# Kernel optimization log

Measured on AMD Instinct MI355X. Metric: run time of the kernel, lower is better.

Reference implementation:

```python
import jax, jax.numpy as jnp
import numpy as np

B, S, H = 2, 2048, 2048
NH, HD = 16, 128


def _rope_tables(seq_len, dim, base=10000.0):
    inv_freq = 1.0 / (base ** (np.arange(0, dim, 2, dtype=np.float32) / dim))
    t = np.arange(seq_len, dtype=np.float32)
    freqs = np.outer(t, inv_freq)                      # [S, dim/2]
    emb = np.concatenate([freqs, freqs], axis=-1)      # [S, dim] (HF convention)
    return jnp.asarray(np.cos(emb)), jnp.asarray(np.sin(emb))


def setup_inputs() -> dict:
    key = jax.random.key(0)
    k1, k2, k3, k4, k5 = jax.random.split(key, 5)
    hidden_states = jax.random.normal(k1, (B, S, H), dtype=jnp.float32)
    # additive causal mask, broadcast over heads: (B, 1, S, S)
    causal = jnp.tril(jnp.ones((S, S), dtype=bool))
    attention_mask = jnp.where(causal, 0.0, -1e9).astype(jnp.float32)
    attention_mask = jnp.broadcast_to(attention_mask[None, None], (B, 1, S, S))
    rope_cos, rope_sin = _rope_tables(S, HD)
    scale = 1.0 / np.sqrt(H)
    Wq = jax.random.normal(k2, (H, H), dtype=jnp.float32) * scale
    Wk = jax.random.normal(k3, (H, H), dtype=jnp.float32) * scale
    Wv = jax.random.normal(k4, (H, H), dtype=jnp.float32) * scale
    Wo = jax.random.normal(k5, (H, H), dtype=jnp.float32) * scale
    return dict(hidden_states=hidden_states, attention_mask=attention_mask,
                rope_cos=rope_cos, rope_sin=rope_sin, Wq=Wq, Wk=Wk, Wv=Wv, Wo=Wo)


def _rotate_half(x):
    half = x.shape[-1] // 2
    return jnp.concatenate([-x[..., half:], x[..., :half]], axis=-1)


def reference(hidden_states, attention_mask, rope_cos, rope_sin, Wq, Wk, Wv, Wo):
    bsz, q_len, _ = hidden_states.shape
    scaling = HD ** -0.5
    # projections (torch Linear: y = x @ W.T)
    q = (hidden_states @ Wq.T).reshape(bsz, q_len, NH, HD).transpose(0, 2, 1, 3)
    k = (hidden_states @ Wk.T).reshape(bsz, q_len, NH, HD).transpose(0, 2, 1, 3)
    v = (hidden_states @ Wv.T).reshape(bsz, q_len, NH, HD).transpose(0, 2, 1, 3)
    # RoPE (rotate_half convention)
    cos = rope_cos[None, None]  # [1,1,S,HD]
    sin = rope_sin[None, None]
    q = q * cos + _rotate_half(q) * sin
    k = k * cos + _rotate_half(k) * sin
    # attention
    scores = jnp.einsum('bhqd,bhkd->bhqk', q, k) * scaling + attention_mask
    attn = jax.nn.softmax(scores.astype(jnp.float32), axis=-1).astype(q.dtype)
    out = jnp.einsum('bhqk,bhkd->bhqd', attn, v)
    out = out.transpose(0, 2, 1, 3).reshape(bsz, q_len, NH * HD)
    return out @ Wo.T
```

## Files before the change

kernel.cpp:

```cpp
#include <hip/hip_runtime.h>
#include <hip/hip_bf16.h>

typedef __bf16 bf16;
typedef __attribute__((ext_vector_type(8))) __bf16 bf16x8;
typedef __attribute__((ext_vector_type(4))) __bf16 bf16x4;
typedef __attribute__((ext_vector_type(4))) float f32x4;

#define BB 2
#define SS 2048
#define HH 2048
#define NH 16
#define HD 128

#define GLOAD_LDS16(g, l)                                                  \
    __builtin_amdgcn_global_load_lds(                                      \
        (const __attribute__((address_space(1))) void*)(g),                \
        (__attribute__((address_space(3))) void*)(l), 16, 0, 0)

__global__ __launch_bounds__(256) void cast_f32_bf16(const float* __restrict__ in,
                                                     bf16* __restrict__ out, int n4) {
    int i = blockIdx.x * 256 + threadIdx.x;
    if (i < n4) {
        f32x4 v = *reinterpret_cast<const f32x4*>(in + (size_t)i * 4);
        bf16x4 o;
        o[0] = (bf16)v[0]; o[1] = (bf16)v[1]; o[2] = (bf16)v[2]; o[3] = (bf16)v[3];
        *reinterpret_cast<bf16x4*>(out + (size_t)i * 4) = o;
    }
}

__global__ __launch_bounds__(512, 2) void gemm256_qkv(const bf16* __restrict__ A,
                                                      const bf16* __restrict__ B,
                                                      bf16* __restrict__ Cb,
                                                      int M, int N, int K) {
    __shared__ bf16 LA[2][256 * 64];
    __shared__ bf16 LB[2][256 * 64];
    const int tid = threadIdx.x, lane = tid & 63, wave = tid >> 6;
    const int l15 = lane & 15, lhi = lane >> 4;
    const int wr = wave >> 2, wc = wave & 3;
    const int NBX = N >> 8;
    const int cpx = gridDim.x >> 3;
    const int wg = (blockIdx.x & 7) * cpx + (blockIdx.x >> 3);
    const int m0 = (wg / NBX) * 256, n0 = (wg % NBX) * 256;
    const int NK = K >> 6;
    const int xor5 = (l15 & 8) << 2;

    auto stageA = [&](int buf, int t, int h) {
        const int k0 = t << 6;
#pragma unroll
        for (int j = 0; j < 2; ++j) {
            int Xw = ((j * 128 + h * 64) << 7) + (wave << 10);
            int X = Xw + lane * 16;
            int T = X ^ (((X >> 10) & 1) << 5);
            GLOAD_LDS16(&A[(size_t)(m0 + (T >> 7)) * K + k0 + ((T & 127) >> 1)],
                        (char*)LA[buf] + Xw);
        }
    };
    auto stageB = [&](int buf, int t, int h) {
        const int k0 = t << 6;
#pragma unroll
        for (int j = 0; j < 2; ++j) {
            int base_row = h * 32 + (2 * j + (wave >> 2)) * 64;
            int Xw = (base_row << 7) + ((wave & 3) << 10);
            int X = Xw + lane * 16;
            int T = X ^ (((X >> 10) & 1) << 5);
            GLOAD_LDS16(&B[(size_t)(n0 + (T >> 7)) * K + k0 + ((T & 127) >> 1)],
                        (char*)LB[buf] + Xw);
        }
    };

    f32x4 acc[8][4] = {};

    stageA(0, 0, 0); stageB(0, 0, 0); stageB(0, 0, 1); stageA(0, 0, 1);
    stageA(1, 1, 0); stageB(1, 1, 1);
    asm volatile("s_waitcnt vmcnt(4)" ::: "memory");
    __builtin_amdgcn_s_barrier();

    bf16x8 af[4][2], bv0[2][2], bv1[2][2];

#pragma unroll 1
    for (int t = 0; t < NK; ++t) {
        const int buf = t & 1;
        char* lA = (char*)LA[buf];
        char* lB = (char*)LB[buf];

#pragma unroll
        for (int f = 0; f < 4; ++f)
#pragma unroll
            for (int ks = 0; ks < 2; ++ks) {
                int T = ((wr * 128 + f * 16 + l15) << 7) + ks * 64 + lhi * 16;
                af[f][ks] = *reinterpret_cast<const bf16x8*>(lA + (T ^ xor5));
            }
#pragma unroll
        for (int g = 0; g < 2; ++g)
#pragma unroll
            for (int ks = 0; ks < 2; ++ks) {
                int T = ((wc * 64 + g * 16 + l15) << 7) + ks * 64 + lhi * 16;
                bv0[g][ks] = *reinterpret_cast<const bf16x8*>(lB + (T ^ xor5));
            }
        if (t + 1 < NK) stageB(buf ^ 1, t + 1, 0);
        __builtin_amdgcn_s_barrier();
        asm volatile("s_waitcnt lgkmcnt(0)" ::: "memory");
        __builtin_amdgcn_s_setprio(1);
#pragma unroll
        for (int f = 0; f < 4; ++f)
#pragma unroll
            for (int g = 0; g < 2; ++g)
#pragma unroll
                for (int ks = 0; ks < 2; ++ks)
                    acc[f][g] = __builtin_amdgcn_mfma_f32_16x16x32_bf16(af[f][ks], bv0[g][ks], acc[f][g], 0, 0, 0);
        __builtin_amdgcn_s_setprio(0);
        __builtin_amdgcn_s_barrier();

#pragma unroll
        for (int g = 0; g < 2; ++g)
#pragma unroll
            for (int ks = 0; ks < 2; ++ks) {
                int T = ((wc * 64 + 32 + g * 16 + l15) << 7) + ks * 64 + lhi * 16;
                bv1[g][ks] = *reinterpret_cast<const bf16x8*>(lB + (T ^ xor5));
            }
        if (t + 1 < NK) stageA(buf ^ 1, t + 1, 1);
        __builtin_amdgcn_s_barrier();
        asm volatile("s_waitcnt lgkmcnt(0)" ::: "memory");
        __builtin_amdgcn_s_setprio(1);
#pragma unroll
        for (int f = 0; f < 4; ++f)
#pragma unroll
            for (int g = 0; g < 2; ++g)
#pragma unroll
                for (int ks = 0; ks < 2; ++ks)
                    acc[f][2 + g] = __builtin_amdgcn_mfma_f32_16x16x32_bf16(af[f][ks], bv1[g][ks], acc[f][2 + g], 0, 0, 0);
        __builtin_amdgcn_s_setprio(0);
        __builtin_amdgcn_s_barrier();

#pragma unroll
        for (int f = 0; f < 4; ++f)
#pragma unroll
            for (int ks = 0; ks < 2; ++ks) {
                int T = ((wr * 128 + 64 + f * 16 + l15) << 7) + ks * 64 + lhi * 16;
                af[f][ks] = *reinterpret_cast<const bf16x8*>(lA + (T ^ xor5));
            }
        if (t + 2 < NK) stageA(buf, t + 2, 0);
        __builtin_amdgcn_s_barrier();
        asm volatile("s_waitcnt lgkmcnt(0)" ::: "memory");
        __builtin_amdgcn_s_setprio(1);
#pragma unroll
        for (int f = 0; f < 4; ++f)
#pragma unroll
            for (int g = 0; g < 2; ++g)
#pragma unroll
                for (int ks = 0; ks < 2; ++ks)
                    acc[4 + f][2 + g] = __builtin_amdgcn_mfma_f32_16x16x32_bf16(af[f][ks], bv1[g][ks], acc[4 + f][2 + g], 0, 0, 0);
        __builtin_amdgcn_s_setprio(0);
        __builtin_amdgcn_s_barrier();

        if (t + 2 < NK) stageB(buf, t + 2, 1);
        __builtin_amdgcn_s_barrier();
        __builtin_amdgcn_s_setprio(1);
#pragma unroll
        for (int f = 0; f < 4; ++f)
#pragma unroll
            for (int g = 0; g < 2; ++g)
#pragma unroll
                for (int ks = 0; ks < 2; ++ks)
                    acc[4 + f][g] = __builtin_amdgcn_mfma_f32_16x16x32_bf16(af[f][ks], bv0[g][ks], acc[4 + f][g], 0, 0, 0);
        __builtin_amdgcn_s_setprio(0);
        if (t + 2 == NK) {
            asm volatile("s_waitcnt vmcnt(0)" ::: "memory");
        } else if (t + 1 < NK) {
            asm volatile("s_waitcnt vmcnt(4)" ::: "memory");
        }
        __builtin_amdgcn_s_barrier();
    }

#pragma unroll
    for (int mf = 0; mf < 8; ++mf)
#pragma unroll
        for (int nf = 0; nf < 4; ++nf)
#pragma unroll
            for (int r = 0; r < 4; ++r) {
                int gm = m0 + wr * 128 + mf * 16 + lhi * 4 + r;
                int gn = n0 + wc * 64 + nf * 16 + l15;
                int proj = gn >> 11, n2 = gn & 2047;
                int b = gm >> 11, s = gm & (SS - 1);
                int h = n2 >> 7, d = n2 & (HD - 1);
                Cb[((size_t)proj << 23) + ((((size_t)(b * NH + h)) * SS + s) << 7) + d] =
                    (bf16)acc[mf][nf][r];
            }
}

__global__ __launch_bounds__(256) void gemm_bt(const bf16* __restrict__ A,
                                               const bf16* __restrict__ B,
                                               float* __restrict__ Cf,
                                               int M, int N, int K) {
    __shared__ bf16 As[128 * 64];
    __shared__ bf16 Bs[128 * 64];
    const int tid = threadIdx.x;
    const int lane = tid & 63, wave = tid >> 6;
    const int l15 = lane & 15, lhi = lane >> 4;
    const int m0 = blockIdx.y * 128, n0 = blockIdx.x * 128;
    const int wm = (wave >> 1) * 64, wn = (wave & 1) * 64;
    const int lrow = lane >> 3;
    const int lcol = (lane & 7) * 8;

    f32x4 acc[4][4] = {};

    for (int k0 = 0; k0 < K; k0 += 64) {
#pragma unroll
        for (int j = 0; j < 4; ++j) {
            const int c = wave * 4 + j;
            const int row = c * 8 + lrow;
            GLOAD_LDS16(&A[(size_t)(m0 + row) * K + k0 + lcol], &As[c * 512]);
            GLOAD_LDS16(&B[(size_t)(n0 + row) * K + k0 + lcol], &Bs[c * 512]);
        }
        __syncthreads();
#pragma unroll
        for (int ks = 0; ks < 2; ++ks) {
            bf16x8 af[4], bfr[4];
#pragma unroll
            for (int i = 0; i < 4; ++i)
                af[i] = *reinterpret_cast<const bf16x8*>(&As[(wm + i * 16 + l15) * 64 + ks * 32 + 8 * lhi]);
#pragma unroll
            for (int j = 0; j < 4; ++j)
                bfr[j] = *reinterpret_cast<const bf16x8*>(&Bs[(wn + j * 16 + l15) * 64 + ks * 32 + 8 * lhi]);
#pragma unroll
            for (int i = 0; i < 4; ++i)
#pragma unroll
                for (int j = 0; j < 4; ++j)
                    acc[i][j] = __builtin_amdgcn_mfma_f32_16x16x32_bf16(af[i], bfr[j], acc[i][j], 0, 0, 0);
        }
        __syncthreads();
    }

#pragma unroll
    for (int i = 0; i < 4; ++i)
#pragma unroll
        for (int j = 0; j < 4; ++j)
#pragma unroll
            for (int r = 0; r < 4; ++r) {
                int gm = m0 + wm + i * 16 + lhi * 4 + r;
                int gn = n0 + wn + j * 16 + l15;
                Cf[(size_t)gm * N + gn] = acc[i][j][r];
            }
}

__global__ __launch_bounds__(256) void transpose_v(const bf16* __restrict__ Vh,
                                                   bf16* __restrict__ Vt) {
    __shared__ bf16 T[64 * 64];
    const int tid = threadIdx.x;
    const int s0 = blockIdx.x * 64, d0 = blockIdx.y * 64, head = blockIdx.z;
    const bf16* src = Vh + ((size_t)head * SS) * HD;
    bf16* dst = Vt + ((size_t)head * HD) * SS;

#pragma unroll
    for (int i = 0; i < 2; ++i) {
        int id = tid + i * 256;
        int r = id >> 3, c16 = id & 7;
        bf16x8 v = *reinterpret_cast<const bf16x8*>(&src[(size_t)(s0 + r) * HD + d0 + c16 * 8]);
        int sw = c16 ^ ((r ^ (r >> 3)) & 7);
        *reinterpret_cast<bf16x8*>((char*)T + r * 128 + sw * 16) = v;
    }
    __syncthreads();
#pragma unroll
    for (int i = 0; i < 2; ++i) {
        int id = tid + i * 256;
        int dr = id >> 3, sc8 = (id & 7) * 8;
        bf16x8 o;
#pragma unroll
        for (int j = 0; j < 8; ++j) {
            int r = sc8 + j;
            int sw = (dr >> 3) ^ ((r ^ (r >> 3)) & 7);
            o[j] = *reinterpret_cast<const bf16*>((char*)T + r * 128 + sw * 16 + (dr & 7) * 2);
        }
        *reinterpret_cast<bf16x8*>(&dst[(size_t)(d0 + dr) * SS + s0 + sc8]) = o;
    }
}

__global__ __launch_bounds__(256) void rope_kernel(bf16* __restrict__ Qh, bf16* __restrict__ Kh,
                                                   const float* __restrict__ cosT,
                                                   const float* __restrict__ sinT) {
    int idx = blockIdx.x * 256 + threadIdx.x;
    int g = idx & 7;
    int s = (idx >> 3) & (SS - 1);
    int head = idx >> 14;
    int d0 = g * 8;
    size_t base = ((size_t)head * SS + s) * HD;
    f32x4 ca = *reinterpret_cast<const f32x4*>(&cosT[s * HD + d0]);
    f32x4 cb = *reinterpret_cast<const f32x4*>(&cosT[s * HD + d0 + 4]);
    f32x4 sa = *reinterpret_cast<const f32x4*>(&sinT[s * HD + d0]);
    f32x4 sb = *reinterpret_cast<const f32x4*>(&sinT[s * HD + d0 + 4]);
    bf16x8 ql = *reinterpret_cast<const bf16x8*>(&Qh[base + d0]);
    bf16x8 qh = *reinterpret_cast<const bf16x8*>(&Qh[base + 64 + d0]);
    bf16x8 kl = *reinterpret_cast<const bf16x8*>(&Kh[base + d0]);
    bf16x8 kh = *reinterpret_cast<const bf16x8*>(&Kh[base + 64 + d0]);
    bf16x8 qlo, qhi, klo, khi;
#pragma unroll
    for (int j = 0; j < 8; ++j) {
        float c = (j < 4) ? ca[j] : cb[j - 4];
        float sn = (j < 4) ? sa[j] : sb[j - 4];
        float q0 = (float)ql[j], q1 = (float)qh[j];
        float k0 = (float)kl[j], k1 = (float)kh[j];
        qlo[j] = (bf16)(q0 * c - q1 * sn);
        qhi[j] = (bf16)(q1 * c + q0 * sn);
        klo[j] = (bf16)(k0 * c - k1 * sn);
        khi[j] = (bf16)(k1 * c + k0 * sn);
    }
    *reinterpret_cast<bf16x8*>(&Qh[base + d0]) = qlo;
    *reinterpret_cast<bf16x8*>(&Qh[base + 64 + d0]) = qhi;
    *reinterpret_cast<bf16x8*>(&Kh[base + d0]) = klo;
    *reinterpret_cast<bf16x8*>(&Kh[base + 64 + d0]) = khi;
}

__global__ __launch_bounds__(256) void attn_kernel(const bf16* __restrict__ Q,
                                                   const bf16* __restrict__ K,
                                                   const bf16* __restrict__ Vt,
                                                   bf16* __restrict__ Ob) {
    __shared__ bf16 Ks[2][64 * 128];
    __shared__ bf16 Vs[2][128 * 64];
    __shared__ bf16 Ps[4][16][72];

    const int tid = threadIdx.x, lane = tid & 63, wave = tid >> 6;
    const int l15 = lane & 15, lhi = lane >> 4;
    const int bid = blockIdx.x;
    const int orig = (bid & 7) * 64 + (bid >> 3);
    const int head = orig >> 4;
    const int pi = orig & 15;
    const int b = head >> 4, h = head & (NH - 1);
    const size_t hb = (size_t)head * SS * HD;
    const bf16* Vth = Vt + (size_t)head * HD * SS;
    const float cexp = 0.08838834764831845f * 1.4426950408889634f;
    const float THR = 62.0f;

#pragma unroll 1
    for (int part = 0; part < 2; ++part) {
        const int t = part ? (31 - pi) : pi;
        const int q0 = t * 64;
        const int qw = q0 + wave * 16;
        const int nkv = t + 1;

        bf16x8 qf[4];
#pragma unroll
        for (int ks = 0; ks < 4; ++ks)
            qf[ks] = *reinterpret_cast<const bf16x8*>(
                &Q[hb + (size_t)(qw + l15) * HD + ks * 32 + 8 * lhi]);

        f32x4 oacc[8] = {};
        float Mr[4], Lp[4];
#pragma unroll
        for (int r = 0; r < 4; ++r) { Mr[r] = -INFINITY; Lp[r] = 0.f; }

        bf16x8 kr[4], vr[4];
#pragma unroll
        for (int i = 0; i < 4; ++i) {
            int id = tid + i * 256;
            kr[i] = *reinterpret_cast<const bf16x8*>(&K[hb + (size_t)(id >> 4) * HD + (id & 15) * 8]);
            vr[i] = *reinterpret_cast<const bf16x8*>(&Vth[(size_t)(id >> 3) * SS + (id & 7) * 8]);
        }
#pragma unroll
        for (int i = 0; i < 4; ++i) {
            int id = tid + i * 256;
            int krow = id >> 4, kc = id & 15;
            *reinterpret_cast<bf16x8*>((char*)Ks[0] + ((krow * 256 + kc * 16) ^ ((krow & 7) << 4))) = kr[i];
            int vrow = id >> 3, vc = id & 7;
            *reinterpret_cast<bf16x8*>((char*)Vs[0] + ((vrow * 128 + vc * 16) ^ ((vrow & 7) << 4))) = vr[i];
        }
        __syncthreads();

        for (int it = 0; it < nkv; ++it) {
            const int cur = it & 1;
            const bool pre = (it + 1 < nkv);
            if (pre) {
                const int kv0 = (it + 1) * 64;
#pragma unroll
                for (int i = 0; i < 4; ++i) {
                    int id = tid + i * 256;
                    kr[i] = *reinterpret_cast<const bf16x8*>(&K[hb + (size_t)(kv0 + (id >> 4)) * HD + (id & 15) * 8]);
                    vr[i] = *reinterpret_cast<const bf16x8*>(&Vth[(size_t)(id >> 3) * SS + kv0 + (id & 7) * 8]);
                }
            }

            f32x4 sf[4] = {};
#pragma unroll
            for (int ks = 0; ks < 4; ++ks) {
#pragma unroll
                for (int ne = 0; ne < 4; ++ne) {
                    int row = ne * 16 + l15;
                    bf16x8 kf = *reinterpret_cast<const bf16x8*>(
                        (const char*)Ks[cur] + ((row * 256 + (ks * 4 + lhi) * 16) ^ ((row & 7) << 4)));
                    sf[ne] = __builtin_amdgcn_mfma_f32_16x16x32_bf16(qf[ks], kf, sf[ne], 0, 0, 0);
                }
            }

            if (it == nkv - 1) {
#pragma unroll
                for (int ne = 0; ne < 4; ++ne)
#pragma unroll
                    for (int r = 0; r < 4; ++r) {
                        int gq = qw + lhi * 4 + r;
                        int gk = it * 64 + ne * 16 + l15;
                        if (gk > gq) sf[ne][r] = -INFINITY;
                    }
            }

            float lm[4];
#pragma unroll
            for (int r = 0; r < 4; ++r)
                lm[r] = fmaxf(fmaxf(sf[0][r], sf[1][r]), fmaxf(sf[2][r], sf[3][r]));
            bool need = (lm[0] > Mr[0] + THR) || (lm[1] > Mr[1] + THR) ||
                        (lm[2] > Mr[2] + THR) || (lm[3] > Mr[3] + THR);
            if (__any(need)) {
                float rmax[4] = {lm[0], lm[1], lm[2], lm[3]};
#pragma unroll
                for (int m = 1; m < 16; m <<= 1)
#pragma unroll
                    for (int r = 0; r < 4; ++r)
                        rmax[r] = fmaxf(rmax[r], __shfl_xor(rmax[r], m));
#pragma unroll
                for (int r = 0; r < 4; ++r) {
                    float nM = fmaxf(Mr[r], rmax[r]);
                    float scf = __builtin_amdgcn_exp2f((Mr[r] - nM) * cexp);
                    Mr[r] = nM;
                    Lp[r] *= scf;
#pragma unroll
                    for (int nf = 0; nf < 8; ++nf) oacc[nf][r] *= scf;
                }
            }
#pragma unroll
            for (int ne = 0; ne < 4; ++ne)
#pragma unroll
                for (int r = 0; r < 4; ++r) {
                    float p = __builtin_amdgcn_exp2f((sf[ne][r] - Mr[r]) * cexp);
                    Lp[r] += p;
                    Ps[wave][lhi * 4 + r][ne * 16 + l15] = (bf16)p;
                }

#pragma unroll
            for (int ks = 0; ks < 2; ++ks) {
                bf16x8 pa = *reinterpret_cast<const bf16x8*>(&Ps[wave][l15][ks * 32 + 8 * lhi]);
#pragma unroll
                for (int nf = 0; nf < 8; ++nf) {
                    int row = nf * 16 + l15;
                    bf16x8 vb = *reinterpret_cast<const bf16x8*>(
                        (const char*)Vs[cur] + ((row * 128 + (ks * 4 + lhi) * 16) ^ ((row & 7) << 4)));
                    oacc[nf] = __builtin_amdgcn_mfma_f32_16x16x32_bf16(pa, vb, oacc[nf], 0, 0, 0);
                }
            }

            if (pre) {
#pragma unroll
                for (int i = 0; i < 4; ++i) {
                    int id = tid + i * 256;
                    int krow = id >> 4, kc = id & 15;
                    *reinterpret_cast<bf16x8*>((char*)Ks[cur ^ 1] + ((krow * 256 + kc * 16) ^ ((krow & 7) << 4))) = kr[i];
                    int vrow = id >> 3, vc = id & 7;
                    *reinterpret_cast<bf16x8*>((char*)Vs[cur ^ 1] + ((vrow * 128 + vc * 16) ^ ((vrow & 7) << 4))) = vr[i];
                }
            }
            __syncthreads();
        }

#pragma unroll
        for (int m = 1; m < 16; m <<= 1)
#pragma unroll
            for (int r = 0; r < 4; ++r)
                Lp[r] += __shfl_xor(Lp[r], m);
        float inv[4];
#pragma unroll
        for (int r = 0; r < 4; ++r) inv[r] = 1.f / Lp[r];
#pragma unroll
        for (int nf = 0; nf < 8; ++nf)
#pragma unroll
            for (int r = 0; r < 4; ++r) {
                int s = qw + lhi * 4 + r;
                int d = nf * 16 + l15;
                Ob[((size_t)(b * SS + s)) * HH + h * HD + d] = (bf16)(oacc[nf][r] * inv[r]);
            }
    }
}

extern "C" void kernel_launch(void* const* d_in, const int* in_sizes, int n_in,
                              void* d_out, int out_size, void* d_ws, size_t ws_size,
                              hipStream_t stream) {
    const float* hs   = (const float*)d_in[0];
    const float* cosT = (const float*)d_in[2];
    const float* sinT = (const float*)d_in[3];
    const float* Wq   = (const float*)d_in[4];
    const float* Wk   = (const float*)d_in[5];
    const float* Wv   = (const float*)d_in[6];
    const float* Wo   = (const float*)d_in[7];
    float* out = (float*)d_out;

    char* w = (char*)d_ws;
    auto alloc = [&](size_t bytes) {
        char* p = w;
        w += (bytes + 255) & ~(size_t)255;
        return p;
    };
    const size_t XE = (size_t)BB * SS * HH;
    const size_t WE = (size_t)HH * HH;
    bf16* Xb   = (bf16*)alloc(XE * 2);
    bf16* Wqkv = (bf16*)alloc(3 * WE * 2);
    bf16* Wob  = (bf16*)alloc(WE * 2);
    bf16* QKV  = (bf16*)alloc(3 * XE * 2);
    bf16* Vtg  = (bf16*)alloc(XE * 2);
    bf16* Ob   = (bf16*)alloc(XE * 2);

    const int M = BB * SS;
    bf16* Qh = QKV;
    bf16* Kh = QKV + XE;
    bf16* Vh = QKV + 2 * XE;

    cast_f32_bf16<<<(int)(XE / 4 + 255) / 256, 256, 0, stream>>>(hs, Xb, (int)(XE / 4));
    cast_f32_bf16<<<(int)(WE / 4 + 255) / 256, 256, 0, stream>>>(Wq, Wqkv, (int)(WE / 4));
    cast_f32_bf16<<<(int)(WE / 4 + 255) / 256, 256, 0, stream>>>(Wk, Wqkv + WE, (int)(WE / 4));
    cast_f32_bf16<<<(int)(WE / 4 + 255) / 256, 256, 0, stream>>>(Wv, Wqkv + 2 * WE, (int)(WE / 4));
    cast_f32_bf16<<<(int)(WE / 4 + 255) / 256, 256, 0, stream>>>(Wo, Wob, (int)(WE / 4));

    gemm256_qkv<<<dim3((M / 256) * (3 * HH / 256)), 512, 0, stream>>>(Xb, Wqkv, QKV, M, 3 * HH, HH);

    rope_kernel<<<(BB * NH * SS * 8) / 256, 256, 0, stream>>>(Qh, Kh, cosT, sinT);

    dim3 tgrid(SS / 64, HD / 64, BB * NH);
    transpose_v<<<tgrid, 256, 0, stream>>>(Vh, Vtg);

    attn_kernel<<<512, 256, 0, stream>>>(Qh, Kh, Vtg, Ob);

    dim3 ogrid(HH / 128, M / 128);
    gemm_bt<<<ogrid, 256, 0, stream>>>(Ob, Wob, out, M, HH, HH);
}
```

Baseline: 320.1 us.

## Fuse five cast launches into one and switch QKV GEMM LDS swizzle

The five separate fp32-to-bf16 cast launches are merged into a single kernel that picks its source and destination buffer by index range, removing four launches and their tail gaps. Separately, the QKV GEMM's LDS swizzle changes from a one-bit XOR on bit 5 to a three-bit XOR of the row index into bits 4-6. Both the global-to-LDS stores and the fragment reads use the new pattern, which spreads 16-byte fragment reads across more LDS banks to cut bank conflicts. The risk is that the staging writes hit new conflicts, or that the index mapping is wrong.

```diff
diff --git a/kernel.cpp b/kernel.cpp
--- a/kernel.cpp
+++ b/kernel.cpp
@@ -17,15 +17,29 @@
         (const __attribute__((address_space(1))) void*)(g),                \
         (__attribute__((address_space(3))) void*)(l), 16, 0, 0)
 
-__global__ __launch_bounds__(256) void cast_f32_bf16(const float* __restrict__ in,
-                                                     bf16* __restrict__ out, int n4) {
+__global__ __launch_bounds__(256) void cast_all(const float* __restrict__ hs,
+                                                const float* __restrict__ Wq,
+                                                const float* __restrict__ Wk,
+                                                const float* __restrict__ Wv,
+                                                const float* __restrict__ Wo,
+                                                bf16* __restrict__ Xb,
+                                                bf16* __restrict__ Wqkv,
+                                                bf16* __restrict__ Wob) {
+    const int XE4 = (BB * SS * HH) / 4;
+    const int WE4 = (HH * HH) / 4;
     int i = blockIdx.x * 256 + threadIdx.x;
-    if (i < n4) {
-        f32x4 v = *reinterpret_cast<const f32x4*>(in + (size_t)i * 4);
-        bf16x4 o;
-        o[0] = (bf16)v[0]; o[1] = (bf16)v[1]; o[2] = (bf16)v[2]; o[3] = (bf16)v[3];
-        *reinterpret_cast<bf16x4*>(out + (size_t)i * 4) = o;
-    }
+    const float* src;
+    bf16* dst;
+    int off;
+    if (i < XE4) { src = hs; dst = Xb; off = i; }
+    else if (i < XE4 + WE4) { src = Wq; dst = Wqkv; off = i - XE4; }
+    else if (i < XE4 + 2 * WE4) { src = Wk; dst = Wqkv + (size_t)HH * HH; off = i - XE4 - WE4; }
+    else if (i < XE4 + 3 * WE4) { src = Wv; dst = Wqkv + 2 * (size_t)HH * HH; off = i - XE4 - 2 * WE4; }
+    else { src = Wo; dst = Wob; off = i - XE4 - 3 * WE4; }
+    f32x4 v = *reinterpret_cast<const f32x4*>(src + (size_t)off * 4);
+    bf16x4 o;
+    o[0] = (bf16)v[0]; o[1] = (bf16)v[1]; o[2] = (bf16)v[2]; o[3] = (bf16)v[3];
+    *reinterpret_cast<bf16x4*>(dst + (size_t)off * 4) = o;
 }
 
 __global__ __launch_bounds__(512, 2) void gemm256_qkv(const bf16* __restrict__ A,
@@ -42,7 +56,7 @@
     const int wg = (blockIdx.x & 7) * cpx + (blockIdx.x >> 3);
     const int m0 = (wg / NBX) * 256, n0 = (wg % NBX) * 256;
     const int NK = K >> 6;
-    const int xor5 = (l15 & 8) << 2;
+    const int xorR = (l15 & 7) << 4;
 
     auto stageA = [&](int buf, int t, int h) {
         const int k0 = t << 6;
@@ -50,7 +64,7 @@
         for (int j = 0; j < 2; ++j) {
             int Xw = ((j * 128 + h * 64) << 7) + (wave << 10);
             int X = Xw + lane * 16;
-            int T = X ^ (((X >> 10) & 1) << 5);
+            int T = X ^ (((X >> 7) & 7) << 4);
             GLOAD_LDS16(&A[(size_t)(m0 + (T >> 7)) * K + k0 + ((T & 127) >> 1)],
                         (char*)LA[buf] + Xw);
         }
@@ -62,7 +76,7 @@
             int base_row = h * 32 + (2 * j + (wave >> 2)) * 64;
             int Xw = (base_row << 7) + ((wave & 3) << 10);
             int X = Xw + lane * 16;
-            int T = X ^ (((X >> 10) & 1) << 5);
+            int T = X ^ (((X >> 7) & 7) << 4);
             GLOAD_LDS16(&B[(size_t)(n0 + (T >> 7)) * K + k0 + ((T & 127) >> 1)],
                         (char*)LB[buf] + Xw);
         }
@@ -88,14 +102,14 @@
 #pragma unroll
             for (int ks = 0; ks < 2; ++ks) {
                 int T = ((wr * 128 + f * 16 + l15) << 7) + ks * 64 + lhi * 16;
-                af[f][ks] = *reinterpret_cast<const bf16x8*>(lA + (T ^ xor5));
+                af[f][ks] = *reinterpret_cast<const bf16x8*>(lA + (T ^ xorR));
             }
 #pragma unroll
         for (int g = 0; g < 2; ++g)
 #pragma unroll
             for (int ks = 0; ks < 2; ++ks) {
                 int T = ((wc * 64 + g * 16 + l15) << 7) + ks * 64 + lhi * 16;
-                bv0[g][ks] = *reinterpret_cast<const bf16x8*>(lB + (T ^ xor5));
+                bv0[g][ks] = *reinterpret_cast<const bf16x8*>(lB + (T ^ xorR));
             }
         if (t + 1 < NK) stageB(buf ^ 1, t + 1, 0);
         __builtin_amdgcn_s_barrier();
@@ -116,7 +130,7 @@
 #pragma unroll
             for (int ks = 0; ks < 2; ++ks) {
                 int T = ((wc * 64 + 32 + g * 16 + l15) << 7) + ks * 64 + lhi * 16;
-                bv1[g][ks] = *reinterpret_cast<const bf16x8*>(lB + (T ^ xor5));
+                bv1[g][ks] = *reinterpret_cast<const bf16x8*>(lB + (T ^ xorR));
             }
         if (t + 1 < NK) stageA(buf ^ 1, t + 1, 1);
         __builtin_amdgcn_s_barrier();
@@ -137,7 +151,7 @@
 #pragma unroll
             for (int ks = 0; ks < 2; ++ks) {
                 int T = ((wr * 128 + 64 + f * 16 + l15) << 7) + ks * 64 + lhi * 16;
-                af[f][ks] = *reinterpret_cast<const bf16x8*>(lA + (T ^ xor5));
+                af[f][ks] = *reinterpret_cast<const bf16x8*>(lA + (T ^ xorR));
             }
         if (t + 2 < NK) stageA(buf, t + 2, 0);
         __builtin_amdgcn_s_barrier();
@@ -509,11 +523,10 @@
     bf16* Kh = QKV + XE;
     bf16* Vh = QKV + 2 * XE;
 
-    cast_f32_bf16<<<(int)(XE / 4 + 255) / 256, 256, 0, stream>>>(hs, Xb, (int)(XE / 4));
-    cast_f32_bf16<<<(int)(WE / 4 + 255) / 256, 256, 0, stream>>>(Wq, Wqkv, (int)(WE / 4));
-    cast_f32_bf16<<<(int)(WE / 4 + 255) / 256, 256, 0, stream>>>(Wk, Wqkv + WE, (int)(WE / 4));
-    cast_f32_bf16<<<(int)(WE / 4 + 255) / 256, 256, 0, stream>>>(Wv, Wqkv + 2 * WE, (int)(WE / 4));
-    cast_f32_bf16<<<(int)(WE / 4 + 255) / 256, 256, 0, stream>>>(Wo, Wob, (int)(WE / 4));
+    {
+        int total4 = (int)((XE + 4 * WE) / 4);
+        cast_all<<<(total4 + 255) / 256, 256, 0, stream>>>(hs, Wq, Wk, Wv, Wo, Xb, Wqkv, Wob);
+    }
 
     gemm256_qkv<<<dim3((M / 256) * (3 * HH / 256)), 512, 0, stream>>>(Xb, Wqkv, QKV, M, 3 * HH, HH);
 
```

After: 301.7 us. -5.7%, faster.
